# Kernel optimization log

Hardware: AMD Instinct MI355X
Metric: run time of the kernel (lower is better)

## Reference

```python
import jax, jax.numpy as jnp
import numpy as np

CODEBOOK_SIZE = 8192
EMBED_DIM = 128
BETA = 0.25


def setup_inputs() -> dict:
    key = jax.random.key(0)
    k1, k2, k3, k4 = jax.random.split(key, 4)
    z = jax.random.normal(k1, (8, 4096, EMBED_DIM), dtype=jnp.float32)
    # nn.Embedding init: normal(0, D**-0.5), frozen
    emb_weight = jax.random.normal(k2, (CODEBOOK_SIZE, EMBED_DIM), dtype=jnp.float32) * (EMBED_DIM ** -0.5)
    # nn.Linear default init scale ~ 1/sqrt(in_features)
    lim = 1.0 / np.sqrt(EMBED_DIM)
    proj_w = jax.random.uniform(k3, (EMBED_DIM, EMBED_DIM), jnp.float32, -lim, lim)
    proj_b = jax.random.uniform(k4, (EMBED_DIM,), jnp.float32, -lim, lim)
    return {"z": z, "emb_weight": emb_weight, "proj_w": proj_w, "proj_b": proj_b}


def reference(z, emb_weight, proj_w, proj_b):
    z_flat = z.reshape(-1, EMBED_DIM)  # [T, D]
    # embedding_proj: Linear -> codebook @ W^T + b
    quant_codebook = emb_weight @ proj_w.T + proj_b  # [K, D]
    # squared distances: |z|^2 + |c|^2 - 2 z c^T  -> [T, K]
    d = (jnp.sum(z_flat ** 2, axis=1, keepdims=True)
         + jnp.sum(quant_codebook ** 2, axis=1)
         - 2.0 * jnp.einsum('td,kd->tk', z_flat, quant_codebook))
    idx = jnp.argmin(d, axis=1)  # [T]
    z_q = quant_codebook[idx].reshape(z.shape)
    # codebook usage / perplexity
    counts = jax.ops.segment_sum(jnp.ones_like(idx, dtype=jnp.float32), idx,
                                 num_segments=CODEBOOK_SIZE)
    e_mean = counts / idx.shape[0]
    perplexity = jnp.exp(-jnp.sum(e_mean * jnp.log(e_mean + 1e-8)))
    sg = jax.lax.stop_gradient
    commit_loss = (BETA * jnp.mean((sg(z_q) - z) ** 2)
                   + jnp.mean((z_q - sg(z)) ** 2))
    z_q_st = z + sg(z_q - z)  # straight-through estimator
    return (z_q_st, commit_loss, perplexity)
```

## Files before the change

### kernel.cpp

```cpp
#include <hip/hip_runtime.h>
#include <math.h>

#define T_TOK 32768
#define D_DIM 128
#define K_CODE 8192
#define BM 512
#define BN 64

typedef unsigned long long ull;
typedef _Float16 v8h __attribute__((ext_vector_type(8)));
typedef _Float16 v4h __attribute__((ext_vector_type(4)));
typedef float v16f __attribute__((ext_vector_type(16)));

#define SCALE 4096.0f
#define DESCALE (1.0f / 4096.0f)
#define ACC_SCALE (-0x1p-23f)


__global__ __launch_bounds__(64) void proj_kernel(const float* __restrict__ E,
                                                  const float* __restrict__ W,
                                                  const float* __restrict__ b,
                                                  char* __restrict__ Cpack,
                                                  float* __restrict__ cn) {
    int r = blockIdx.x;
    int l = threadIdx.x;
    const float4* E4 = (const float4*)(E + (size_t)r * D_DIM);
    const float4* WA = (const float4*)(W + (size_t)l * D_DIM);
    const float4* WB = (const float4*)(W + (size_t)(l + 64) * D_DIM);

    float4 aA = make_float4(0.f, 0.f, 0.f, 0.f);
    float4 aB = make_float4(0.f, 0.f, 0.f, 0.f);
#pragma unroll
    for (int dd = 0; dd < 32; ++dd) {
        float4 e = E4[dd];
        float4 wa = WA[dd], wb = WB[dd];
        aA.x = fmaf(e.x, wa.x, aA.x);
        aA.y = fmaf(e.y, wa.y, aA.y);
        aA.z = fmaf(e.z, wa.z, aA.z);
        aA.w = fmaf(e.w, wa.w, aA.w);
        aB.x = fmaf(e.x, wb.x, aB.x);
        aB.y = fmaf(e.y, wb.y, aB.y);
        aB.z = fmaf(e.z, wb.z, aB.z);
        aB.w = fmaf(e.w, wb.w, aB.w);
    }
    float vA = ((aA.x + aA.y) + (aA.z + aA.w)) + b[l];
    float vB = ((aB.x + aB.y) + (aB.z + aB.w)) + b[l + 64];

    char* cp = Cpack + (size_t)(r >> 6) * 32768;
    int mt = (r >> 5) & 1, rs = r & 31;
    {
        int kc = l >> 4, hf = (l >> 3) & 1, j = l & 7;
        float f = vA * SCALE;
        _Float16 h = (_Float16)f;
        _Float16 m = (_Float16)(f - (float)h);
        size_t off = (size_t)((mt * 8 + kc) * 1024 + (hf * 32 + rs) * 16 + j * 2);
        *(_Float16*)(cp + off) = h;
        *(_Float16*)(cp + off + 16384) = m;
    }
    {
        int d = l + 64;
        int kc = d >> 4, hf = (d >> 3) & 1, j = d & 7;
        float f = vB * SCALE;
        _Float16 h = (_Float16)f;
        _Float16 m = (_Float16)(f - (float)h);
        size_t off = (size_t)((mt * 8 + kc) * 1024 + (hf * 32 + rs) * 16 + j * 2);
        *(_Float16*)(cp + off) = h;
        *(_Float16*)(cp + off + 16384) = m;
    }

    float s = vA * vA + vB * vB;
#pragma unroll
    for (int off = 32; off > 0; off >>= 1) s += __shfl_down(s, off, 64);
    if (l == 0) cn[r] = s;
}

__global__ __launch_bounds__(64) void znorm_kernel(const float* __restrict__ Z,
                                                   float* __restrict__ zn,
                                                   ull* __restrict__ packed,
                                                   int* __restrict__ counts,
                                                   float* __restrict__ loss) {
    int t = blockIdx.x;
    int l = threadIdx.x;
    float a = Z[(size_t)t * D_DIM + l];
    float b2 = Z[(size_t)t * D_DIM + 64 + l];
    float s = a * a + b2 * b2;
#pragma unroll
    for (int off = 32; off > 0; off >>= 1) s += __shfl_down(s, off, 64);
    if (l == 0) {
        zn[t] = s;
        packed[t] = ~0ull;
        if (t < K_CODE) counts[t] = 0;
        if (t == 0) loss[0] = 0.f;
    }
}

__global__ __launch_bounds__(256) void prep_z_kernel(const float* __restrict__ Z,
                                                     char* __restrict__ Zpack) {
    int tb = blockIdx.x;
    int tid = threadIdx.x;
    int lane = tid & 63;
    int w = tid >> 6;
    char* zp = Zpack + (size_t)tb * 16384;
#pragma unroll
    for (int kq = 0; kq < 2; ++kq) {
        int kc = 2 * w + kq;
        const float* src = Z + (size_t)(tb * 32 + (lane & 31)) * D_DIM
                             + kc * 16 + (lane >> 5) * 8;
        float4 a = *(const float4*)(src);
        float4 c = *(const float4*)(src + 4);
        float vals[8] = {a.x, a.y, a.z, a.w, c.x, c.y, c.z, c.w};
        v8h h, m;
#pragma unroll
        for (int j = 0; j < 8; ++j) {
            float f = vals[j] * SCALE;
            _Float16 hh = (_Float16)f;
            h[j] = hh;
            m[j] = (_Float16)(f - (float)hh);
        }
        *(v8h*)(zp + (size_t)(kc * 1024 + lane * 16)) = h;
        *(v8h*)(zp + (size_t)(8192 + kc * 1024 + lane * 16)) = m;
    }
}

__global__ __launch_bounds__(256, 2) void argmin_kernel(const char* __restrict__ Zpack,
                                                        const char* __restrict__ Cpack,
                                                        const float* __restrict__ cn,
                                                        const float* __restrict__ zn,
                                                        ull* __restrict__ packed) {
    __shared__ char lds[33024];

    int tid = threadIdx.x;
    int lane = tid & 63;
    int w = __builtin_amdgcn_readfirstlane(tid >> 6);
    int cb = blockIdx.x;
    int nb = cb * BN;
    int mb = blockIdx.y * BM;

    {
        const float4* src = (const float4*)(Cpack + (size_t)cb * 32768);
        float4* dst = (float4*)lds;
#pragma unroll
        for (int it = 0; it < 8; ++it) dst[it * 256 + tid] = src[it * 256 + tid];
        if (tid < 64) *(float*)(lds + 32768 + tid * 4) = cn[nb + tid];
    }
    __syncthreads();

    v16f acc[2][4];
#pragma unroll
    for (int mt = 0; mt < 2; ++mt)
#pragma unroll
        for (int n = 0; n < 4; ++n) acc[mt][n] = (v16f)0.f;

    int tbw = (mb >> 5) + 4 * w;
    const char* zb0 = Zpack + (size_t)tbw * 16384 + lane * 16;
    const char* ab = lds + lane * 16;

    v8h pb[8][2];
#pragma unroll
    for (int n = 0; n < 4; ++n) {
        pb[2 * n + 0][0] = *(const v8h*)(zb0 + n * 16384);
        pb[2 * n + 1][0] = *(const v8h*)(zb0 + n * 16384 + 8192);
        pb[2 * n + 0][1] = *(const v8h*)(zb0 + n * 16384 + 1024);
        pb[2 * n + 1][1] = *(const v8h*)(zb0 + n * 16384 + 8192 + 1024);
    }

#pragma unroll
    for (int kc = 0; kc < 8; ++kc) {
        int cur = kc & 1;
        v8h Bh[4], Bm[4];
#pragma unroll
        for (int n = 0; n < 4; ++n) { Bh[n] = pb[2 * n][cur]; Bm[n] = pb[2 * n + 1][cur]; }
        if (kc < 6) {
#pragma unroll
            for (int n = 0; n < 4; ++n) {
                pb[2 * n + 0][cur] = *(const v8h*)(zb0 + n * 16384 + (kc + 2) * 1024);
                pb[2 * n + 1][cur] = *(const v8h*)(zb0 + n * 16384 + 8192 + (kc + 2) * 1024);
            }
        }
        v8h Ah0 = *(const v8h*)(ab + (0 * 8 + kc) * 1024);
        v8h Ah1 = *(const v8h*)(ab + (1 * 8 + kc) * 1024);
        v8h Am0 = *(const v8h*)(ab + (2 * 8 + kc) * 1024);
        v8h Am1 = *(const v8h*)(ab + (3 * 8 + kc) * 1024);

#pragma unroll
        for (int n = 0; n < 4; ++n)
            acc[0][n] = __builtin_amdgcn_mfma_f32_32x32x16_f16(Ah0, Bh[n], acc[0][n], 0, 0, 0);
#pragma unroll
        for (int n = 0; n < 4; ++n)
            acc[1][n] = __builtin_amdgcn_mfma_f32_32x32x16_f16(Ah1, Bh[n], acc[1][n], 0, 0, 0);
#pragma unroll
        for (int n = 0; n < 4; ++n)
            acc[0][n] = __builtin_amdgcn_mfma_f32_32x32x16_f16(Ah0, Bm[n], acc[0][n], 0, 0, 0);
#pragma unroll
        for (int n = 0; n < 4; ++n)
            acc[1][n] = __builtin_amdgcn_mfma_f32_32x32x16_f16(Ah1, Bm[n], acc[1][n], 0, 0, 0);
#pragma unroll
        for (int n = 0; n < 4; ++n)
            acc[0][n] = __builtin_amdgcn_mfma_f32_32x32x16_f16(Am0, Bh[n], acc[0][n], 0, 0, 0);
#pragma unroll
        for (int n = 0; n < 4; ++n)
            acc[1][n] = __builtin_amdgcn_mfma_f32_32x32x16_f16(Am1, Bh[n], acc[1][n], 0, 0, 0);
    }

    const float* cn_s = (const float*)(lds + 32768);
    int half_id = lane >> 5;

#pragma unroll
    for (int n = 0; n < 4; ++n) {
        int tok = mb + w * 128 + n * 32 + (lane & 31);
        float znv = zn[tok];
        float best = 3.4e38f;
        int bi = nb;
#pragma unroll
        for (int mt = 0; mt < 2; ++mt) {
#pragma unroll
            for (int reg = 0; reg < 16; ++reg) {
                int mrow = 32 * mt + (reg & 3) + 8 * (reg >> 2) + 4 * half_id;
                float cnv = cn_s[mrow];
                int code = nb + mrow;
                float s = fmaf(acc[mt][n][reg], ACC_SCALE, znv + cnv);
                if (s < best) { best = s; bi = code; }
            }
        }
        float ob = __shfl_xor(best, 32, 64);
        int oi = __shfl_xor(bi, 32, 64);
        if (ob < best || (ob == best && oi < bi)) { best = ob; bi = oi; }
        if ((n >> 1) == half_id) {
            ull pk = ((ull)__float_as_uint(best) << 32) | (unsigned)bi;
            atomicMin(&packed[tok], pk);
        }
    }
}

__global__ __launch_bounds__(256) void zq_kernel(const float* __restrict__ Z,
                                                 const char* __restrict__ Cpack,
                                                 const ull* __restrict__ packed,
                                                 float* __restrict__ out,
                                                 int* __restrict__ counts,
                                                 float* __restrict__ loss) {
    int gid = blockIdx.x * 256 + threadIdx.x;
    int t = gid >> 5;
    int d4 = gid & 31;
    int idx = (int)(packed[t] & 0xFFFFFFFFull);
    if (d4 == 0) atomicAdd(&counts[idx], 1);

    int d0 = 4 * d4;
    int kc = d0 >> 4, hf = (d0 >> 3) & 1, j0 = d0 & 7;
    const char* cp = Cpack + (size_t)(idx >> 6) * 32768
                   + (size_t)((((idx >> 5) & 1) * 8 + kc) * 1024
                              + (hf * 32 + (idx & 31)) * 16 + j0 * 2);
    v4h h = *(const v4h*)(cp);
    v4h m = *(const v4h*)(cp + 16384);
    float4 cv;
    cv.x = ((float)h[0] + (float)m[0]) * DESCALE;
    cv.y = ((float)h[1] + (float)m[1]) * DESCALE;
    cv.z = ((float)h[2] + (float)m[2]) * DESCALE;
    cv.w = ((float)h[3] + (float)m[3]) * DESCALE;

    float4 zv = ((const float4*)Z)[gid];
    float dx = cv.x - zv.x, dy = cv.y - zv.y, dz = cv.z - zv.z, dw = cv.w - zv.w;
    float4 o;
    o.x = zv.x + dx;
    o.y = zv.y + dy;
    o.z = zv.z + dz;
    o.w = zv.w + dw;
    ((float4*)out)[gid] = o;

    float ls = dx * dx + dy * dy + dz * dz + dw * dw;
#pragma unroll
    for (int off = 32; off > 0; off >>= 1) ls += __shfl_down(ls, off, 64);
    __shared__ float red[4];
    int lane = threadIdx.x & 63, w = threadIdx.x >> 6;
    if (lane == 0) red[w] = ls;
    __syncthreads();
    if (threadIdx.x == 0) {
        atomicAdd(loss, (red[0] + red[1]) + (red[2] + red[3]));
    }
}

__global__ __launch_bounds__(256) void scalars_kernel(const int* __restrict__ counts,
                                                      const float* __restrict__ loss,
                                                      float* __restrict__ out) {
    float s = 0.f;
    for (int i = threadIdx.x; i < K_CODE; i += 256) {
        float e = (float)counts[i] * (1.0f / (float)T_TOK);
        s += e * logf(e + 1e-8f);
    }
#pragma unroll
    for (int off = 32; off > 0; off >>= 1) s += __shfl_down(s, off, 64);
    __shared__ float red[4];
    int lane = threadIdx.x & 63, w = threadIdx.x >> 6;
    if (lane == 0) red[w] = s;
    __syncthreads();
    if (threadIdx.x == 0) {
        float ssum = (red[0] + red[1]) + (red[2] + red[3]);
        out[(size_t)T_TOK * D_DIM + 0] = 1.25f * loss[0] / (float)((size_t)T_TOK * D_DIM);
        out[(size_t)T_TOK * D_DIM + 1] = expf(-ssum);
    }
}

extern "C" void kernel_launch(void* const* d_in, const int* in_sizes, int n_in,
                              void* d_out, int out_size, void* d_ws, size_t ws_size,
                              hipStream_t stream) {
    const float* z   = (const float*)d_in[0];
    const float* emb = (const float*)d_in[1];
    const float* pw  = (const float*)d_in[2];
    const float* pb  = (const float*)d_in[3];
    float* out = (float*)d_out;

    char* Zpack = (char*)d_out;

    char* ws = (char*)d_ws;
    char*  Cpack  = ws + 0;
    float* cn     = (float*)(ws + 4194304);
    float* zn     = (float*)(ws + 4227072);
    ull*   packed = (ull*)  (ws + 4358144);
    int*   counts = (int*)  (ws + 4620288);
    float* loss   = (float*)(ws + 4653056);

    proj_kernel<<<K_CODE, 64, 0, stream>>>(emb, pw, pb, Cpack, cn);
    prep_z_kernel<<<T_TOK / 32, 256, 0, stream>>>(z, Zpack);
    znorm_kernel<<<T_TOK, 64, 0, stream>>>(z, zn, packed, counts, loss);
    argmin_kernel<<<dim3(K_CODE / BN, T_TOK / BM), 256, 0, stream>>>(Zpack, Cpack, cn, zn, packed);
    zq_kernel<<<(T_TOK * D_DIM / 4) / 256, 256, 0, stream>>>(z, Cpack, packed, out, counts, loss);
    scalars_kernel<<<1, 256, 0, stream>>>(counts, loss, out);
}
```

Baseline: 407.3 us.

## Loop argmin blocks over codebook tiles with async double-buffered LDS staging

```diff
diff --git a/kernel.cpp b/kernel.cpp
--- a/kernel.cpp
+++ b/kernel.cpp
@@ -6,6 +6,7 @@
 #define K_CODE 8192
 #define BM 512
 #define BN 64
+#define NTILE 8
 
 typedef unsigned long long ull;
 typedef _Float16 v8h __attribute__((ext_vector_type(8)));
@@ -17,13 +18,13 @@
 #define ACC_SCALE (-0x1p-23f)
 
 
-__global__ __launch_bounds__(64) void proj_kernel(const float* __restrict__ E,
+__global__ __launch_bounds__(256) void proj_kernel(const float* __restrict__ E,
                                                   const float* __restrict__ W,
                                                   const float* __restrict__ b,
                                                   char* __restrict__ Cpack,
                                                   float* __restrict__ cn) {
-    int r = blockIdx.x;
-    int l = threadIdx.x;
+    int r = blockIdx.x * 4 + (threadIdx.x >> 6);
+    int l = threadIdx.x & 63;
     const float4* E4 = (const float4*)(E + (size_t)r * D_DIM);
     const float4* WA = (const float4*)(W + (size_t)l * D_DIM);
     const float4* WB = (const float4*)(W + (size_t)(l + 64) * D_DIM);
@@ -74,13 +75,12 @@
     if (l == 0) cn[r] = s;
 }
 
-__global__ __launch_bounds__(64) void znorm_kernel(const float* __restrict__ Z,
+__global__ __launch_bounds__(256) void znorm_kernel(const float* __restrict__ Z,
                                                    float* __restrict__ zn,
                                                    ull* __restrict__ packed,
-                                                   int* __restrict__ counts,
-                                                   float* __restrict__ loss) {
-    int t = blockIdx.x;
-    int l = threadIdx.x;
+                                                   int* __restrict__ counts) {
+    int t = blockIdx.x * 4 + (threadIdx.x >> 6);
+    int l = threadIdx.x & 63;
     float a = Z[(size_t)t * D_DIM + l];
     float b2 = Z[(size_t)t * D_DIM + 64 + l];
     float s = a * a + b2 * b2;
@@ -90,7 +90,6 @@
         zn[t] = s;
         packed[t] = ~0ull;
         if (t < K_CODE) counts[t] = 0;
-        if (t == 0) loss[0] = 0.f;
     }
 }
 
@@ -122,38 +121,45 @@
     }
 }
 
+__device__ __forceinline__ void stage_tile(char* ldsdst, const char* gsrc,
+                                           int w, int lane) {
+#pragma unroll
+    for (int it = 0; it < 8; ++it) {
+        int off = (w * 8 + it) * 1024;
+        __builtin_amdgcn_global_load_lds(
+            (const __attribute__((address_space(1))) void*)(gsrc + off + lane * 16),
+            (__attribute__((address_space(3))) void*)(ldsdst + off),
+            16, 0, 0);
+    }
+}
+
 __global__ __launch_bounds__(256, 2) void argmin_kernel(const char* __restrict__ Zpack,
                                                         const char* __restrict__ Cpack,
                                                         const float* __restrict__ cn,
                                                         const float* __restrict__ zn,
                                                         ull* __restrict__ packed) {
-    __shared__ char lds[33024];
+    __shared__ __align__(16) char lds[2][32768];
 
     int tid = threadIdx.x;
     int lane = tid & 63;
     int w = __builtin_amdgcn_readfirstlane(tid >> 6);
-    int cb = blockIdx.x;
-    int nb = cb * BN;
+    int half_id = lane >> 5;
+    int cb0 = blockIdx.x * NTILE;
     int mb = blockIdx.y * BM;
-
-    {
-        const float4* src = (const float4*)(Cpack + (size_t)cb * 32768);
-        float4* dst = (float4*)lds;
-#pragma unroll
-        for (int it = 0; it < 8; ++it) dst[it * 256 + tid] = src[it * 256 + tid];
-        if (tid < 64) *(float*)(lds + 32768 + tid * 4) = cn[nb + tid];
-    }
-    __syncthreads();
-
-    v16f acc[2][4];
-#pragma unroll
-    for (int mt = 0; mt < 2; ++mt)
-#pragma unroll
-        for (int n = 0; n < 4; ++n) acc[mt][n] = (v16f)0.f;
 
     int tbw = (mb >> 5) + 4 * w;
     const char* zb0 = Zpack + (size_t)tbw * 16384 + lane * 16;
-    const char* ab = lds + lane * 16;
+
+    stage_tile(&lds[0][0], Cpack + (size_t)cb0 * 32768, w, lane);
+
+    float znv[4];
+#pragma unroll
+    for (int n = 0; n < 4; ++n) znv[n] = zn[mb + w * 128 + n * 32 + (lane & 31)];
+
+    float best[4];
+    int bi[4];
+#pragma unroll
+    for (int n = 0; n < 4; ++n) { best[n] = 3.4e38f; bi[n] = 0; }
 
     v8h pb[8][2];
 #pragma unroll
@@ -164,69 +170,94 @@
         pb[2 * n + 1][1] = *(const v8h*)(zb0 + n * 16384 + 8192 + 1024);
     }
 
-#pragma unroll
-    for (int kc = 0; kc < 8; ++kc) {
-        int cur = kc & 1;
-        v8h Bh[4], Bm[4];
-#pragma unroll
-        for (int n = 0; n < 4; ++n) { Bh[n] = pb[2 * n][cur]; Bm[n] = pb[2 * n + 1][cur]; }
-        if (kc < 6) {
+    __syncthreads();
+
+#pragma unroll 1
+    for (int j = 0; j < NTILE; ++j) {
+        const char* ab = &lds[j & 1][0] + lane * 16;
+
+        v16f acc[2][4];
+#pragma unroll
+        for (int mt = 0; mt < 2; ++mt)
+#pragma unroll
+            for (int n = 0; n < 4; ++n) acc[mt][n] = (v16f)0.f;
+
+#pragma unroll
+        for (int kc = 0; kc < 8; ++kc) {
+            int curb = kc & 1;
+            v8h Bh[4], Bm[4];
+#pragma unroll
+            for (int n = 0; n < 4; ++n) { Bh[n] = pb[2 * n][curb]; Bm[n] = pb[2 * n + 1][curb]; }
+            {
+                int knx = (kc + 2) & 7;
+#pragma unroll
+                for (int n = 0; n < 4; ++n) {
+                    pb[2 * n + 0][curb] = *(const v8h*)(zb0 + n * 16384 + knx * 1024);
+                    pb[2 * n + 1][curb] = *(const v8h*)(zb0 + n * 16384 + 8192 + knx * 1024);
+                }
+            }
+            v8h Ah0 = *(const v8h*)(ab + (0 * 8 + kc) * 1024);
+            v8h Ah1 = *(const v8h*)(ab + (1 * 8 + kc) * 1024);
+            v8h Am0 = *(const v8h*)(ab + (2 * 8 + kc) * 1024);
+            v8h Am1 = *(const v8h*)(ab + (3 * 8 + kc) * 1024);
+
+#pragma unroll
+            for (int n = 0; n < 4; ++n)
+                acc[0][n] = __builtin_amdgcn_mfma_f32_32x32x16_f16(Ah0, Bh[n], acc[0][n], 0, 0, 0);
+#pragma unroll
+            for (int n = 0; n < 4; ++n)
+                acc[1][n] = __builtin_amdgcn_mfma_f32_32x32x16_f16(Ah1, Bh[n], acc[1][n], 0, 0, 0);
+#pragma unroll
+            for (int n = 0; n < 4; ++n)
+                acc[0][n] = __builtin_amdgcn_mfma_f32_32x32x16_f16(Ah0, Bm[n], acc[0][n], 0, 0, 0);
+#pragma unroll
+            for (int n = 0; n < 4; ++n)
+                acc[1][n] = __builtin_amdgcn_mfma_f32_32x32x16_f16(Ah1, Bm[n], acc[1][n], 0, 0, 0);
+#pragma unroll
+            for (int n = 0; n < 4; ++n)
+                acc[0][n] = __builtin_amdgcn_mfma_f32_32x32x16_f16(Am0, Bh[n], acc[0][n], 0, 0, 0);
+#pragma unroll
+            for (int n = 0; n < 4; ++n)
+                acc[1][n] = __builtin_amdgcn_mfma_f32_32x32x16_f16(Am1, Bh[n], acc[1][n], 0, 0, 0);
+        }
+
+        if (j + 1 < NTILE)
+            stage_tile(&lds[(j + 1) & 1][0],
+                       Cpack + (size_t)(cb0 + j + 1) * 32768, w, lane);
+
+        int nb = (cb0 + j) * BN;
+        const float* cnp = cn + nb;
+#pragma unroll
+        for (int mt = 0; mt < 2; ++mt) {
+            float cnreg[16];
+#pragma unroll
+            for (int reg = 0; reg < 16; ++reg) {
+                int mrow = 32 * mt + (reg & 3) + 8 * (reg >> 2) + 4 * half_id;
+                cnreg[reg] = cnp[mrow];
+            }
 #pragma unroll
             for (int n = 0; n < 4; ++n) {
-                pb[2 * n + 0][cur] = *(const v8h*)(zb0 + n * 16384 + (kc + 2) * 1024);
-                pb[2 * n + 1][cur] = *(const v8h*)(zb0 + n * 16384 + 8192 + (kc + 2) * 1024);
+#pragma unroll
+                for (int reg = 0; reg < 16; ++reg) {
+                    int mrow = 32 * mt + (reg & 3) + 8 * (reg >> 2) + 4 * half_id;
+                    int code = nb + mrow;
+                    float s = fmaf(acc[mt][n][reg], ACC_SCALE, znv[n] + cnreg[reg]);
+                    if (s < best[n]) { best[n] = s; bi[n] = code; }
+                }
             }
         }
-        v8h Ah0 = *(const v8h*)(ab + (0 * 8 + kc) * 1024);
-        v8h Ah1 = *(const v8h*)(ab + (1 * 8 + kc) * 1024);
-        v8h Am0 = *(const v8h*)(ab + (2 * 8 + kc) * 1024);
-        v8h Am1 = *(const v8h*)(ab + (3 * 8 + kc) * 1024);
-
-#pragma unroll
-        for (int n = 0; n < 4; ++n)
-            acc[0][n] = __builtin_amdgcn_mfma_f32_32x32x16_f16(Ah0, Bh[n], acc[0][n], 0, 0, 0);
-#pragma unroll
-        for (int n = 0; n < 4; ++n)
-            acc[1][n] = __builtin_amdgcn_mfma_f32_32x32x16_f16(Ah1, Bh[n], acc[1][n], 0, 0, 0);
-#pragma unroll
-        for (int n = 0; n < 4; ++n)
-            acc[0][n] = __builtin_amdgcn_mfma_f32_32x32x16_f16(Ah0, Bm[n], acc[0][n], 0, 0, 0);
-#pragma unroll
-        for (int n = 0; n < 4; ++n)
-            acc[1][n] = __builtin_amdgcn_mfma_f32_32x32x16_f16(Ah1, Bm[n], acc[1][n], 0, 0, 0);
-#pragma unroll
-        for (int n = 0; n < 4; ++n)
-            acc[0][n] = __builtin_amdgcn_mfma_f32_32x32x16_f16(Am0, Bh[n], acc[0][n], 0, 0, 0);
-#pragma unroll
-        for (int n = 0; n < 4; ++n)
-            acc[1][n] = __builtin_amdgcn_mfma_f32_32x32x16_f16(Am1, Bh[n], acc[1][n], 0, 0, 0);
-    }
-
-    const float* cn_s = (const float*)(lds + 32768);
-    int half_id = lane >> 5;
+
+        __syncthreads();
+    }
 
 #pragma unroll
     for (int n = 0; n < 4; ++n) {
-        int tok = mb + w * 128 + n * 32 + (lane & 31);
-        float znv = zn[tok];
-        float best = 3.4e38f;
-        int bi = nb;
-#pragma unroll
-        for (int mt = 0; mt < 2; ++mt) {
-#pragma unroll
-            for (int reg = 0; reg < 16; ++reg) {
-                int mrow = 32 * mt + (reg & 3) + 8 * (reg >> 2) + 4 * half_id;
-                float cnv = cn_s[mrow];
-                int code = nb + mrow;
-                float s = fmaf(acc[mt][n][reg], ACC_SCALE, znv + cnv);
-                if (s < best) { best = s; bi = code; }
-            }
-        }
-        float ob = __shfl_xor(best, 32, 64);
-        int oi = __shfl_xor(bi, 32, 64);
-        if (ob < best || (ob == best && oi < bi)) { best = ob; bi = oi; }
+        float ob = __shfl_xor(best[n], 32, 64);
+        int oi = __shfl_xor(bi[n], 32, 64);
+        if (ob < best[n] || (ob == best[n] && oi < bi[n])) { best[n] = ob; bi[n] = oi; }
         if ((n >> 1) == half_id) {
-            ull pk = ((ull)__float_as_uint(best) << 32) | (unsigned)bi;
+            int tok = mb + w * 128 + n * 32 + (lane & 31);
+            ull pk = ((ull)__float_as_uint(best[n]) << 32) | (unsigned)bi[n];
             atomicMin(&packed[tok], pk);
         }
     }
@@ -237,7 +268,7 @@
                                                  const ull* __restrict__ packed,
                                                  float* __restrict__ out,
                                                  int* __restrict__ counts,
-                                                 float* __restrict__ loss) {
+                                                 float* __restrict__ lpart) {
     int gid = blockIdx.x * 256 + threadIdx.x;
     int t = gid >> 5;
     int d4 = gid & 31;
@@ -273,28 +304,32 @@
     int lane = threadIdx.x & 63, w = threadIdx.x >> 6;
     if (lane == 0) red[w] = ls;
     __syncthreads();
-    if (threadIdx.x == 0) {
-        atomicAdd(loss, (red[0] + red[1]) + (red[2] + red[3]));
-    }
+    if (threadIdx.x == 0) lpart[blockIdx.x] = (red[0] + red[1]) + (red[2] + red[3]);
 }
 
 __global__ __launch_bounds__(256) void scalars_kernel(const int* __restrict__ counts,
-                                                      const float* __restrict__ loss,
+                                                      const float* __restrict__ lpart,
                                                       float* __restrict__ out) {
     float s = 0.f;
     for (int i = threadIdx.x; i < K_CODE; i += 256) {
         float e = (float)counts[i] * (1.0f / (float)T_TOK);
         s += e * logf(e + 1e-8f);
     }
-#pragma unroll
-    for (int off = 32; off > 0; off >>= 1) s += __shfl_down(s, off, 64);
-    __shared__ float red[4];
+    float ls = 0.f;
+    for (int i = threadIdx.x; i < 4096; i += 256) ls += lpart[i];
+#pragma unroll
+    for (int off = 32; off > 0; off >>= 1) {
+        s += __shfl_down(s, off, 64);
+        ls += __shfl_down(ls, off, 64);
+    }
+    __shared__ float red[8];
     int lane = threadIdx.x & 63, w = threadIdx.x >> 6;
-    if (lane == 0) red[w] = s;
+    if (lane == 0) { red[w] = s; red[4 + w] = ls; }
     __syncthreads();
     if (threadIdx.x == 0) {
         float ssum = (red[0] + red[1]) + (red[2] + red[3]);
-        out[(size_t)T_TOK * D_DIM + 0] = 1.25f * loss[0] / (float)((size_t)T_TOK * D_DIM);
+        float lsum = (red[4] + red[5]) + (red[6] + red[7]);
+        out[(size_t)T_TOK * D_DIM + 0] = 1.25f * lsum / (float)((size_t)T_TOK * D_DIM);
         out[(size_t)T_TOK * D_DIM + 1] = expf(-ssum);
     }
 }
@@ -316,12 +351,12 @@
     float* zn     = (float*)(ws + 4227072);
     ull*   packed = (ull*)  (ws + 4358144);
     int*   counts = (int*)  (ws + 4620288);
-    float* loss   = (float*)(ws + 4653056);
-
-    proj_kernel<<<K_CODE, 64, 0, stream>>>(emb, pw, pb, Cpack, cn);
+    float* lpart  = (float*)(ws + 4227072);
+
+    proj_kernel<<<K_CODE / 4, 256, 0, stream>>>(emb, pw, pb, Cpack, cn);
     prep_z_kernel<<<T_TOK / 32, 256, 0, stream>>>(z, Zpack);
-    znorm_kernel<<<T_TOK, 64, 0, stream>>>(z, zn, packed, counts, loss);
-    argmin_kernel<<<dim3(K_CODE / BN, T_TOK / BM), 256, 0, stream>>>(Zpack, Cpack, cn, zn, packed);
-    zq_kernel<<<(T_TOK * D_DIM / 4) / 256, 256, 0, stream>>>(z, Cpack, packed, out, counts, loss);
-    scalars_kernel<<<1, 256, 0, stream>>>(counts, loss, out);
-}
+    znorm_kernel<<<T_TOK / 4, 256, 0, stream>>>(z, zn, packed, counts);
+    argmin_kernel<<<dim3(K_CODE / BN / NTILE, T_TOK / BM), 256, 0, stream>>>(Zpack, Cpack, cn, zn, packed);
+    zq_kernel<<<(T_TOK * D_DIM / 4) / 256, 256, 0, stream>>>(z, Cpack, packed, out, counts, lpart);
+    scalars_kernel<<<1, 256, 0, stream>>>(counts, lpart, out);
+}
```

After: 480.7 us. 18.0% more time.
